# Performance work log

Measured on AMD Instinct MI355X. Metric: run time of the kernel, lower is better.

The kernel has to match this reference:

```python
import jax, jax.numpy as jnp
import numpy as np

B = 16      # number of point clouds
N = 4096    # points per cloud (max segment size, static)
D = 3       # xyz


def setup_inputs() -> dict:
    key = jax.random.key(0)
    k1, k2 = jax.random.split(key)
    pred = jax.random.normal(k1, (B * N, D), dtype=jnp.float32)
    target = jax.random.normal(k2, (B * N, D), dtype=jnp.float32)
    # sorted batch assignment with equal-size segments (so N_max is static)
    batch = jnp.repeat(jnp.arange(B, dtype=jnp.int64), N)
    return {"pred": pred, "target": target, "batch": batch}


def _to_dense_batch(x, batch):
    # Faithful to torch_geometric.utils.to_dense_batch: scatter each point into
    # its (cloud, within-cloud-position) slot; padding slots stay zero.
    T = x.shape[0]
    counts = jax.ops.segment_sum(jnp.ones((T,), jnp.int32), batch, num_segments=B)
    starts = jnp.concatenate([jnp.zeros((1,), jnp.int32), jnp.cumsum(counts)[:-1]])
    pos = jnp.arange(T, dtype=jnp.int32) - starts[batch]
    dense = jnp.zeros((B, N, x.shape[1]), x.dtype).at[batch, pos].set(x)
    return dense


def _chamfer(x, y):
    # pytorch3d.loss.chamfer_distance defaults: squared L2, point_reduction="mean",
    # batch_reduction="mean"; no lengths -> padded zeros count as points (as in source).
    x2 = jnp.sum(x * x, axis=-1)                      # [B, N]
    y2 = jnp.sum(y * y, axis=-1)                      # [B, N]
    xy = jnp.einsum("bid,bjd->bij", x, y)             # [B, N, N]
    d2 = x2[:, :, None] + y2[:, None, :] - 2.0 * xy   # [B, N, N] squared dists
    cham_x = jnp.mean(jnp.min(d2, axis=2), axis=1)    # x -> nearest y, mean over points
    cham_y = jnp.mean(jnp.min(d2, axis=1), axis=1)    # y -> nearest x
    return jnp.mean(cham_x + cham_y)                  # batch mean of summed directions


def reference(pred, target, batch):
    dense_x = _to_dense_batch(pred, batch)
    dense_y = _to_dense_batch(target, batch)
    return _chamfer(dense_x, dense_y)
```

## Files before the change

### kernel.cpp

```cpp
#include <hip/hip_runtime.h>


typedef __attribute__((ext_vector_type(8))) short bf16x8;
typedef __attribute__((ext_vector_type(16))) float floatx16;

#define BB 16
#define NN 4096
#define T  256
#define NPTS (BB * NN)
#define YC 512
#define NC (NN / YC)
#define XC 128
#define NXB (NN / XC)
#define NBLK (2 * BB * NXB)
#define ONEBF 0x3F80u

__device__ __forceinline__ unsigned int f2bf(float f) {
    unsigned int u = __float_as_uint(f);
    u += 0x7fffu + ((u >> 16) & 1u);
    return u >> 16;
}
__device__ __forceinline__ float bf2f(unsigned int h) {
    return __uint_as_float(h << 16);
}

__global__ __launch_bounds__(T) void chamfer_prep(
    const float* __restrict__ pred, const float* __restrict__ target,
    uint4* __restrict__ rec0, uint4* __restrict__ rec1)
{
    int g = blockIdx.x * T + threadIdx.x;
    int set = g >> 16;
    int idx = g & (NPTS - 1);
    const float* yp = (set ? pred : target) + (size_t)idx * 3;
    float y0 = yp[0], y1 = yp[1], y2 = yp[2];
    unsigned int h0 = f2bf(y0), h1 = f2bf(y1), h2 = f2bf(y2);
    unsigned int H0 = f2bf(-2.f * bf2f(h0));
    unsigned int H1 = f2bf(-2.f * bf2f(h1));
    unsigned int H2 = f2bf(-2.f * bf2f(h2));
    unsigned int L0 = f2bf(-2.f * (y0 - bf2f(h0)));
    unsigned int L1 = f2bf(-2.f * (y1 - bf2f(h1)));
    unsigned int L2 = f2bf(-2.f * (y2 - bf2f(h2)));
    float ysq = fmaf(y0, y0, fmaf(y1, y1, y2 * y2));
    unsigned int sh = f2bf(ysq);
    unsigned int sl = f2bf(ysq - bf2f(sh));
    rec0[g] = make_uint4(H0 | (H1 << 16), H2 | (H0 << 16),
                         H1 | (H2 << 16), L0 | (L1 << 16));
    rec1[g] = make_uint4(L2 | (ONEBF << 16), ONEBF | (sh << 16),
                         sl, 0u);
}

__global__ __launch_bounds__(T, 2) void chamfer_main(
    const float* __restrict__ pred, const float* __restrict__ target,
    const uint4* __restrict__ rec0, const uint4* __restrict__ rec1,
    float* __restrict__ bsum)
{
    __shared__ uint4 ldsy[2][YC];
    __shared__ float wsum[4];

    const int xb  = blockIdx.x;
    const int b   = blockIdx.y;
    const int dir = blockIdx.z;
    const float* xsrc = (dir ? target : pred) + (size_t)b * NN * 3;
    const size_t ygbase = (size_t)dir * NPTS + (size_t)b * NN;
    const int tid  = threadIdx.x;
    const int lane = tid & 63, w = tid >> 6;
    const int kg   = lane >> 5, m = lane & 31;

    union U { uint4 q; bf16x8 v; };
    U au;
    {
        int xi = xb * XC + w * 32 + m;
        const float* xp = xsrc + (size_t)xi * 3;
        float x0 = xp[0], x1 = xp[1], x2 = xp[2];
        unsigned int h0 = f2bf(x0), h1 = f2bf(x1), h2 = f2bf(x2);
        unsigned int L0 = f2bf(x0 - bf2f(h0));
        unsigned int L1 = f2bf(x1 - bf2f(h1));
        unsigned int L2 = f2bf(x2 - bf2f(h2));
        float xsq = fmaf(x0, x0, fmaf(x1, x1, x2 * x2));
        unsigned int sh = f2bf(xsq);
        unsigned int sl = f2bf(xsq - bf2f(sh));
        au.q = make_uint4(kg ? (h2 | (sh << 16))    : (h0 | (h1 << 16)),
                          kg ? (sl | (ONEBF << 16)) : (h2 | (L0 << 16)),
                          kg ? ONEBF                : (L1 | (L2 << 16)),
                          kg ? 0u                   : (h0 | (h1 << 16)));
    }

    floatx16 acc, zacc;
#pragma unroll
    for (int r = 0; r < 16; ++r) { acc[r] = 3.402823466e38f; zacc[r] = 0.f; }

    for (int c = 0; c < NC; ++c) {
        __syncthreads();
        for (int i = tid; i < YC; i += T) {
            ldsy[0][i] = rec0[ygbase + c * YC + i];
            ldsy[1][i] = rec1[ygbase + c * YC + i];
        }
        __syncthreads();
#pragma unroll 2
        for (int t = 0; t < YC / 32; t += 2) {
            U bu0, bu1;
            bu0.q = ldsy[kg][t * 32 + m];
            bu1.q = ldsy[kg][t * 32 + 32 + m];
            floatx16 d0 = __builtin_amdgcn_mfma_f32_32x32x16_bf16(
                au.v, bu0.v, zacc, 0, 0, 0);
            floatx16 d1 = __builtin_amdgcn_mfma_f32_32x32x16_bf16(
                au.v, bu1.v, zacc, 0, 0, 0);
#pragma unroll
            for (int r = 0; r < 16; ++r)
                acc[r] = fminf(fminf(acc[r], d0[r]), d1[r]);
        }
    }

    float s = 0.f;
#pragma unroll
    for (int r = 0; r < 16; ++r) {
        float v = acc[r];
        v = fminf(v, __shfl_xor(v, 1, 64));
        v = fminf(v, __shfl_xor(v, 2, 64));
        v = fminf(v, __shfl_xor(v, 4, 64));
        v = fminf(v, __shfl_xor(v, 8, 64));
        v = fminf(v, __shfl_xor(v, 16, 64));
        s += fmaxf(v, 0.f);
    }
    s += __shfl_xor(s, 32, 64);
    if (lane == 0) wsum[w] = s;
    __syncthreads();
    if (tid == 0)
        bsum[(dir * BB + b) * NXB + xb] = wsum[0] + wsum[1] + wsum[2] + wsum[3];
}

__global__ __launch_bounds__(T) void chamfer_final(
    const float* __restrict__ bsum, float* __restrict__ out)
{
    float s = 0.f;
    for (int i = threadIdx.x; i < NBLK; i += T) s += bsum[i];
#pragma unroll
    for (int off = 32; off > 0; off >>= 1)
        s += __shfl_down(s, off, 64);
    __shared__ float wsum[4];
    if ((threadIdx.x & 63) == 0) wsum[threadIdx.x >> 6] = s;
    __syncthreads();
    if (threadIdx.x == 0)
        out[0] = (wsum[0] + wsum[1] + wsum[2] + wsum[3]) * (1.0f / (BB * NN));
}

extern "C" void kernel_launch(void* const* d_in, const int* in_sizes, int n_in,
                              void* d_out, int out_size, void* d_ws, size_t ws_size,
                              hipStream_t stream) {
    const float* pred   = (const float*)d_in[0];
    const float* target = (const float*)d_in[1];
    float* out  = (float*)d_out;
    uint4* rec0 = (uint4*)d_ws;
    uint4* rec1 = rec0 + 2 * NPTS;
    float* bsum = (float*)(rec1 + 2 * NPTS);

    chamfer_prep<<<2 * NPTS / T, T, 0, stream>>>(pred, target, rec0, rec1);
    dim3 grid(NXB, BB, 2);
    chamfer_main<<<grid, T, 0, stream>>>(pred, target, rec0, rec1, bsum);
    chamfer_final<<<1, T, 0, stream>>>(bsum, out);
}
```

Measured before the change: 84.56 us.

## Register-block four x tiles per wave, split y range, double-buffer LDS

Each wave now holds four 32-row x fragments, so every B fragment read from LDS feeds four MFMAs instead of one. The y range is split in two across the grid to keep the block count up, and per-row partial minima are written to a buffer that a parallel final kernel combines with atomicAdd. The y chunks are double-buffered: the next chunk is loaded into registers while the current one is computed, which removes one barrier per chunk. In exchange, register pressure rises (four accumulators of 16 floats each) and there is an extra memset plus a global round trip for the row minima.

```diff
diff --git a/kernel.cpp b/kernel.cpp
--- a/kernel.cpp
+++ b/kernel.cpp
@@ -8,11 +8,13 @@
 #define NN 4096
 #define T  256
 #define NPTS (BB * NN)
+#define RS 4
+#define XC (4 * RS * 32)
+#define NXB (NN / XC)
+#define YS 2
+#define YH (NN / YS)
 #define YC 512
-#define NC (NN / YC)
-#define XC 128
-#define NXB (NN / XC)
-#define NBLK (2 * BB * NXB)
+#define NC (YH / YC)
 #define ONEBF 0x3F80u
 
 __device__ __forceinline__ unsigned int f2bf(float f) {
@@ -52,24 +54,25 @@
 __global__ __launch_bounds__(T, 2) void chamfer_main(
     const float* __restrict__ pred, const float* __restrict__ target,
     const uint4* __restrict__ rec0, const uint4* __restrict__ rec1,
-    float* __restrict__ bsum)
+    float* __restrict__ rowp)
 {
-    __shared__ uint4 ldsy[2][YC];
-    __shared__ float wsum[4];
+    __shared__ uint4 ldsy[2][2][YC];
 
     const int xb  = blockIdx.x;
     const int b   = blockIdx.y;
-    const int dir = blockIdx.z;
+    const int dir = blockIdx.z >> 1;
+    const int ys  = blockIdx.z & 1;
     const float* xsrc = (dir ? target : pred) + (size_t)b * NN * 3;
-    const size_t ygbase = (size_t)dir * NPTS + (size_t)b * NN;
+    const size_t ygbase = (size_t)dir * NPTS + (size_t)b * NN + (size_t)ys * YH;
     const int tid  = threadIdx.x;
     const int lane = tid & 63, w = tid >> 6;
     const int kg   = lane >> 5, m = lane & 31;
 
     union U { uint4 q; bf16x8 v; };
-    U au;
-    {
-        int xi = xb * XC + w * 32 + m;
+    U au[RS];
+#pragma unroll
+    for (int s = 0; s < RS; ++s) {
+        int xi = xb * XC + w * (RS * 32) + s * 32 + m;
         const float* xp = xsrc + (size_t)xi * 3;
         float x0 = xp[0], x1 = xp[1], x2 = xp[2];
         unsigned int h0 = f2bf(x0), h1 = f2bf(x1), h2 = f2bf(x2);
@@ -79,69 +82,106 @@
         float xsq = fmaf(x0, x0, fmaf(x1, x1, x2 * x2));
         unsigned int sh = f2bf(xsq);
         unsigned int sl = f2bf(xsq - bf2f(sh));
-        au.q = make_uint4(kg ? (h2 | (sh << 16))    : (h0 | (h1 << 16)),
-                          kg ? (sl | (ONEBF << 16)) : (h2 | (L0 << 16)),
-                          kg ? ONEBF                : (L1 | (L2 << 16)),
-                          kg ? 0u                   : (h0 | (h1 << 16)));
-    }
-
-    floatx16 acc, zacc;
-#pragma unroll
-    for (int r = 0; r < 16; ++r) { acc[r] = 3.402823466e38f; zacc[r] = 0.f; }
+        au[s].q = make_uint4(kg ? (h2 | (sh << 16))    : (h0 | (h1 << 16)),
+                             kg ? (sl | (ONEBF << 16)) : (h2 | (L0 << 16)),
+                             kg ? ONEBF                : (L1 | (L2 << 16)),
+                             kg ? 0u                   : (h0 | (h1 << 16)));
+    }
+
+    floatx16 acc[RS], zacc;
+#pragma unroll
+    for (int r = 0; r < 16; ++r) zacc[r] = 0.f;
+#pragma unroll
+    for (int s = 0; s < RS; ++s)
+#pragma unroll
+        for (int r = 0; r < 16; ++r) acc[s][r] = 3.402823466e38f;
+
+    ldsy[0][0][tid]     = rec0[ygbase + tid];
+    ldsy[0][0][T + tid] = rec0[ygbase + T + tid];
+    ldsy[0][1][tid]     = rec1[ygbase + tid];
+    ldsy[0][1][T + tid] = rec1[ygbase + T + tid];
+    __syncthreads();
 
     for (int c = 0; c < NC; ++c) {
+        const int cur = c & 1, nxt = cur ^ 1;
+        uint4 s0a, s0b, s1a, s1b;
+        if (c + 1 < NC) {
+            size_t base = ygbase + (size_t)(c + 1) * YC;
+            s0a = rec0[base + tid];
+            s0b = rec0[base + T + tid];
+            s1a = rec1[base + tid];
+            s1b = rec1[base + T + tid];
+        }
+        U b0, b1;
+        b0.q = ldsy[cur][kg][m];
+        b1.q = ldsy[cur][kg][32 + m];
+#pragma unroll 2
+        for (int p = 0; p < YC / 64; ++p) {
+            U n0, n1;
+            int q = (p + 1) & 7;
+            n0.q = ldsy[cur][kg][q * 64 + m];
+            n1.q = ldsy[cur][kg][q * 64 + 32 + m];
+#pragma unroll
+            for (int s = 0; s < RS; ++s) {
+                floatx16 d0 = __builtin_amdgcn_mfma_f32_32x32x16_bf16(
+                    au[s].v, b0.v, zacc, 0, 0, 0);
+                floatx16 d1 = __builtin_amdgcn_mfma_f32_32x32x16_bf16(
+                    au[s].v, b1.v, zacc, 0, 0, 0);
+#pragma unroll
+                for (int r = 0; r < 16; ++r)
+                    acc[s][r] = fminf(fminf(acc[s][r], d0[r]), d1[r]);
+            }
+            b0 = n0; b1 = n1;
+        }
+        if (c + 1 < NC) {
+            ldsy[nxt][0][tid]     = s0a;
+            ldsy[nxt][0][T + tid] = s0b;
+            ldsy[nxt][1][tid]     = s1a;
+            ldsy[nxt][1][T + tid] = s1b;
+        }
         __syncthreads();
-        for (int i = tid; i < YC; i += T) {
-            ldsy[0][i] = rec0[ygbase + c * YC + i];
-            ldsy[1][i] = rec1[ygbase + c * YC + i];
-        }
-        __syncthreads();
-#pragma unroll 2
-        for (int t = 0; t < YC / 32; t += 2) {
-            U bu0, bu1;
-            bu0.q = ldsy[kg][t * 32 + m];
-            bu1.q = ldsy[kg][t * 32 + 32 + m];
-            floatx16 d0 = __builtin_amdgcn_mfma_f32_32x32x16_bf16(
-                au.v, bu0.v, zacc, 0, 0, 0);
-            floatx16 d1 = __builtin_amdgcn_mfma_f32_32x32x16_bf16(
-                au.v, bu1.v, zacc, 0, 0, 0);
-#pragma unroll
-            for (int r = 0; r < 16; ++r)
-                acc[r] = fminf(fminf(acc[r], d0[r]), d1[r]);
-        }
-    }
-
-    float s = 0.f;
-#pragma unroll
-    for (int r = 0; r < 16; ++r) {
-        float v = acc[r];
-        v = fminf(v, __shfl_xor(v, 1, 64));
-        v = fminf(v, __shfl_xor(v, 2, 64));
-        v = fminf(v, __shfl_xor(v, 4, 64));
-        v = fminf(v, __shfl_xor(v, 8, 64));
-        v = fminf(v, __shfl_xor(v, 16, 64));
-        s += fmaxf(v, 0.f);
-    }
-    s += __shfl_xor(s, 32, 64);
-    if (lane == 0) wsum[w] = s;
-    __syncthreads();
-    if (tid == 0)
-        bsum[(dir * BB + b) * NXB + xb] = wsum[0] + wsum[1] + wsum[2] + wsum[3];
+    }
+
+    float* rp = rowp + ((size_t)((dir * BB + b) * YS + ys)) * NN + xb * XC;
+#pragma unroll
+    for (int s = 0; s < RS; ++s) {
+#pragma unroll
+        for (int r = 0; r < 16; ++r) {
+            float v = acc[s][r];
+            v = fminf(v, __shfl_xor(v, 1, 64));
+            v = fminf(v, __shfl_xor(v, 2, 64));
+            v = fminf(v, __shfl_xor(v, 4, 64));
+            v = fminf(v, __shfl_xor(v, 8, 64));
+            v = fminf(v, __shfl_xor(v, 16, 64));
+            if (m == 0) {
+                int row = (r & 3) + 8 * (r >> 2) + 4 * kg;
+                rp[w * (RS * 32) + s * 32 + row] = v;
+            }
+        }
+    }
 }
 
 __global__ __launch_bounds__(T) void chamfer_final(
-    const float* __restrict__ bsum, float* __restrict__ out)
+    const float* __restrict__ rowp, float* __restrict__ out)
 {
     float s = 0.f;
-    for (int i = threadIdx.x; i < NBLK; i += T) s += bsum[i];
+    for (int e = blockIdx.x * T + threadIdx.x; e < 2 * BB * NN;
+         e += gridDim.x * T) {
+        int g = e >> 12, x = e & (NN - 1);
+        float v = fminf(rowp[(size_t)(2 * g) * NN + x],
+                        rowp[(size_t)(2 * g + 1) * NN + x]);
+        s += fmaxf(v, 0.f);
+    }
 #pragma unroll
     for (int off = 32; off > 0; off >>= 1)
         s += __shfl_down(s, off, 64);
     __shared__ float wsum[4];
     if ((threadIdx.x & 63) == 0) wsum[threadIdx.x >> 6] = s;
     __syncthreads();
-    if (threadIdx.x == 0)
-        out[0] = (wsum[0] + wsum[1] + wsum[2] + wsum[3]) * (1.0f / (BB * NN));
+    if (threadIdx.x == 0) {
+        float t = wsum[0] + wsum[1] + wsum[2] + wsum[3];
+        atomicAdd(out, t * (1.0f / (BB * NN)));
+    }
 }
 
 extern "C" void kernel_launch(void* const* d_in, const int* in_sizes, int n_in,
@@ -152,10 +192,11 @@
     float* out  = (float*)d_out;
     uint4* rec0 = (uint4*)d_ws;
     uint4* rec1 = rec0 + 2 * NPTS;
-    float* bsum = (float*)(rec1 + 2 * NPTS);
-
+    float* rowp = (float*)(rec1 + 2 * NPTS);
+
+    hipMemsetAsync(out, 0, sizeof(float), stream);
     chamfer_prep<<<2 * NPTS / T, T, 0, stream>>>(pred, target, rec0, rec1);
-    dim3 grid(NXB, BB, 2);
-    chamfer_main<<<grid, T, 0, stream>>>(pred, target, rec0, rec1, bsum);
-    chamfer_final<<<1, T, 0, stream>>>(bsum, out);
-}
+    dim3 grid(NXB, BB, 2 * YS);
+    chamfer_main<<<grid, T, 0, stream>>>(pred, target, rec0, rec1, rowp);
+    chamfer_final<<<128, T, 0, stream>>>(rowp, out);
+}
```

Result: slower. 95.74 us (+13.2%).
